# Performance work log

Hardware: AMD Instinct MI355X
Metric: run time of the kernel (lower is better)

## Reference

```python
import jax, jax.numpy as jnp
import numpy as np
import math

D = 128       # d_model (file-scope constant)
L_LEN = 128   # length; forced == d_model by the un-transposed attention call
NH = 4        # n_head
DK = D // NH
K = 7         # depthwise conv kernel size
LC = 4        # conv_num
EPS = 1e-5    # LayerNorm eps
NEG = -1e30


def _pos_encoding():
    i = np.arange(D).astype(np.float64)
    freqs = np.where(i % 2 == 0, 10000.0 ** (-i / D), -(10000.0 ** ((1 - i) / D)))
    phases = np.where(i % 2 == 0, 0.0, math.pi / 2)
    pos = np.arange(L_LEN).astype(np.float64)[None, :]          # (1, L)
    pe = np.sin(pos * freqs[:, None] + phases[:, None])          # (D, L)
    return jnp.asarray(pe, jnp.float32)

PE = _pos_encoding()


def layernorm2d(x, w, b):
    # LayerNorm over the trailing (D, L) dims jointly, elementwise affine (D, L)
    mu = x.mean(axis=(-2, -1), keepdims=True)
    var = x.var(axis=(-2, -1), keepdims=True)
    return (x - mu) * jax.lax.rsqrt(var + EPS) * w + b


def sep_conv(x, dw_w, dw_b, pw_w, pw_b):
    # depthwise conv1d (groups=C) then 1x1 pointwise conv. x: (B, C, L)
    h = jax.lax.conv_general_dilated(
        x, dw_w[:, None, :], window_strides=(1,), padding=[(K // 2, K // 2)],
        dimension_numbers=('NCH', 'OIH', 'NCH'), feature_group_count=D)
    h = h + dw_b[:, None]
    return jnp.einsum('bcl,oc->bol', h, pw_w) + pw_b[:, None]


def mha(x, mask_f, Wq, bq, Wk, bk, Wv, bv, Wo, bo):
    # x: (B, Lx, F) with Lx == F == D here (module feeds (B, d_model, length) untransposed)
    B, Lx, _ = x.shape
    q = (x @ Wq.T + bq).reshape(B, Lx, NH, DK)
    k = (x @ Wk.T + bk).reshape(B, Lx, NH, DK)
    v = (x @ Wv.T + bv).reshape(B, Lx, NH, DK)
    scores = jnp.einsum('bqhd,bkhd->bhqk', q, k) * (1.0 / math.sqrt(DK))
    m = mask_f[:, None, None, :]                         # (B,1,1,Lx)
    scores = scores * (1.0 - m) + m * NEG                # mask_logits
    attn = jax.nn.softmax(scores, axis=-1)
    out = jnp.einsum('bhqk,bkhd->bqhd', attn, v).reshape(B, Lx, D)
    return out @ Wo.T + bo


def setup_inputs() -> dict:
    key = jax.random.key(0)
    ks = jax.random.split(key, 16)
    B = 1024
    s = 0.02
    inp = {
        'x': jax.random.normal(ks[0], (B, D, L_LEN), jnp.float32),
        'mask': jax.random.randint(ks[1], (B, L_LEN), 0, 2, jnp.int32),
        'dw_w': jax.random.normal(ks[2], (LC, D, K), jnp.float32) * s,
        'dw_b': jnp.zeros((LC, D), jnp.float32),
        'pw_w': jax.random.normal(ks[3], (LC, D, D), jnp.float32) * s,
        'pw_b': jnp.zeros((LC, D), jnp.float32),
        'normb_w': jnp.ones((D, L_LEN), jnp.float32),
        'normb_b': jnp.zeros((D, L_LEN), jnp.float32),
        'norms_w': jnp.ones((LC, D, L_LEN), jnp.float32),
        'norms_b': jnp.zeros((LC, D, L_LEN), jnp.float32),
        'norme_w': jnp.ones((D, L_LEN), jnp.float32),
        'norme_b': jnp.zeros((D, L_LEN), jnp.float32),
        'Wq': jax.random.normal(ks[4], (D, D), jnp.float32) * s,
        'bq': jnp.zeros((D,), jnp.float32),
        'Wk': jax.random.normal(ks[5], (D, D), jnp.float32) * s,
        'bk': jnp.zeros((D,), jnp.float32),
        'Wv': jax.random.normal(ks[6], (D, D), jnp.float32) * s,
        'bv': jnp.zeros((D,), jnp.float32),
        'Wo': jax.random.normal(ks[7], (D, D), jnp.float32) * s,
        'bo': jnp.zeros((D,), jnp.float32),
        'fc_w': jax.random.normal(ks[8], (D, D), jnp.float32) * s,
        'fc_b': jnp.zeros((D,), jnp.float32),
    }
    return inp


def reference(x, mask, dw_w, dw_b, pw_w, pw_b, normb_w, normb_b, norms_w, norms_b,
              norme_w, norme_b, Wq, bq, Wk, bk, Wv, bv, Wo, bo, fc_w, fc_b):
    # Eval mode: all dropouts are identity.
    mask_f = mask.astype(x.dtype)
    out = x + PE                                  # PosEncoder
    res = out
    out = layernorm2d(out, normb_w, normb_b)      # normb
    for i in range(LC):                           # fixed small layer loop
        h = sep_conv(out, dw_w[i], dw_b[i], pw_w[i], pw_b[i])
        out = jax.nn.relu(h) + res
        res = out
        out = layernorm2d(out, norms_w[i], norms_b[i])
    att = mha(out, mask_f, Wq, bq, Wk, bk, Wv, bv, Wo, bo)
    out = att + res
    res = out
    out = layernorm2d(out, norme_w, norme_b)
    # fc applied over channel dim: (B,C,L)->(B,L,C) linear ->(B,C,L)
    h = jnp.einsum('bcl,oc->bol', out, fc_w) + fc_b[:, None]
    out = jax.nn.relu(h) + res
    return out
```

## Files before the change

kernel.cpp:

```cpp
#include <hip/hip_runtime.h>

#define NEGF -1e30f
#define EPSF 1e-5f

typedef __attribute__((ext_vector_type(8))) short bf16x8;
typedef __attribute__((ext_vector_type(4))) float f32x4;
typedef unsigned short u16;
typedef unsigned int u32;

#define WSU_PW 0
#define WSU_FC 65536
#define WSU_WO 81920
#define WSU_WQ 98304
#define WSU_WK 114688
#define WSU_WV 131072
#define WSU_END 147456

__device__ __forceinline__ u16 f2bf(float x) {
  u32 u = __float_as_uint(x);
  u += 0x7fffu + ((u >> 16) & 1u);
  return (u16)(u >> 16);
}
__device__ __forceinline__ float bf2f(u16 u) {
  return __uint_as_float(((u32)u) << 16);
}
__device__ __forceinline__ f32x4 mfma16(bf16x8 a, bf16x8 b, f32x4 c) {
  return __builtin_amdgcn_mfma_f32_16x16x32_bf16(a, b, c, 0, 0, 0);
}

__global__ __launch_bounds__(128) void prep_kernel(
    const float* __restrict__ pw_w, const float* __restrict__ fc_w,
    const float* __restrict__ Wo, const float* __restrict__ Wq,
    const float* __restrict__ Wk, const float* __restrict__ Wv,
    u16* __restrict__ wsu) {
  int job = blockIdx.x, r = blockIdx.y, c = threadIdx.x;
  int idx = r * 128 + c;
  if (job < 4)       wsu[WSU_PW + job * 16384 + idx] = f2bf(pw_w[job * 16384 + idx]);
  else if (job == 4) wsu[WSU_FC + idx] = f2bf(fc_w[idx]);
  else if (job == 5) wsu[WSU_WO + idx] = f2bf(Wo[idx]);
  else if (job == 6) wsu[WSU_WQ + idx] = f2bf(Wq[idx]);
  else if (job == 7) wsu[WSU_WK + idx] = f2bf(Wk[idx]);
  else if (job == 8) wsu[WSU_WV + idx] = f2bf(Wv[idx]);
  else {
    float* pe = (float*)(wsu + WSU_END);
    int d = r, pos = c;
    double freq, phase;
    if ((d & 1) == 0) { freq = pow(10000.0, -(double)d / 128.0); phase = 0.0; }
    else { freq = -pow(10000.0, (1.0 - (double)d) / 128.0); phase = 1.5707963267948966; }
    pe[d * 128 + pos] = (float)sin((double)pos * freq + phase);
  }
}

__device__ __forceinline__ void ln_stats(const float* resv, float* red, int t,
                                         float& mu, float& inv) {
  float s = 0.f, s2 = 0.f;
#pragma unroll
  for (int i = 0; i < 32; i++) { float v = resv[i]; s += v; s2 += v * v; }
#pragma unroll
  for (int off = 32; off > 0; off >>= 1) {
    s += __shfl_down(s, off, 64);
    s2 += __shfl_down(s2, off, 64);
  }
  if ((t & 63) == 0) { red[(t >> 6) * 2] = s; red[(t >> 6) * 2 + 1] = s2; }
  __syncthreads();
  float S = 0.f, S2 = 0.f;
#pragma unroll
  for (int i = 0; i < 8; i++) { S += red[2 * i]; S2 += red[2 * i + 1]; }
  mu = S * (1.0f / 16384.0f);
  float var = S2 * (1.0f / 16384.0f) - mu * mu;
  inv = rsqrtf(var + EPSF);
}

__global__ __launch_bounds__(512, 4) void enc_kernel(
    const float* __restrict__ x, const int* __restrict__ mask,
    const float* __restrict__ dw_w, const float* __restrict__ dw_b,
    const float* __restrict__ pw_b,
    const float* __restrict__ normb_w, const float* __restrict__ normb_b,
    const float* __restrict__ norms_w, const float* __restrict__ norms_b,
    const float* __restrict__ norme_w, const float* __restrict__ norme_b,
    const float* __restrict__ bq, const float* __restrict__ bk,
    const float* __restrict__ bv, const float* __restrict__ bo,
    const float* __restrict__ fc_b, const u16* __restrict__ wsu,
    const float* __restrict__ pe, float* __restrict__ out) {
  __shared__ __align__(16) u16 A_raw[128 * 136 + 16];
  __shared__ __align__(16) u16 B_[128 * 136];
  __shared__ float mask_s[128];
  __shared__ float red[16];
  u16* A = A_raw + 8;
  u16* QH = B_;
  u16* KH = B_ + 5120;
  u16* VT = B_ + 10240;
  u16* PN = B_;

  const int t = threadIdx.x;
  const int b = blockIdx.x;
  const int lane = t & 63;
  const int r16 = lane & 15;
  const int quad = lane >> 4;
  const int m0 = __builtin_amdgcn_readfirstlane((t >> 6) << 4);
  const int l = t & 127;
  const int obase = __builtin_amdgcn_readfirstlane((t >> 7) << 5);
  const int dw_o = t & 127;
  const int dw_seg = __builtin_amdgcn_readfirstlane(t >> 7);

  if (t < 128) mask_s[t] = (float)mask[b * 128 + t];

  float res[32];
  {
    const float* xb = x + (size_t)b * 16384;
#pragma unroll
    for (int i = 0; i < 32; i++) {
      int o = obase + i;
      res[i] = xb[o * 128 + l] + pe[o * 128 + l];
    }
  }
  {
    float mu, inv;
    ln_stats(res, red, t, mu, inv);
#pragma unroll
    for (int i = 0; i < 32; i++) {
      int o = obase + i;
      A[o * 136 + l] = f2bf((res[i] - mu) * inv * normb_w[o * 128 + l] + normb_b[o * 128 + l]);
    }
    __syncthreads();
  }

#pragma unroll 1
  for (int layer = 0; layer < 4; layer++) {
    {
      const float* dwp = dw_w + layer * 896 + dw_o * 7;
      float wreg[7];
#pragma unroll
      for (int j = 0; j < 7; j++) wreg[j] = dwp[j];
      float bias = dw_b[layer * 128 + dw_o];
      const u16* xrow = A + dw_o * 136;
#pragma unroll
      for (int k = 0; k < 4; k++) {
        const int lb = dw_seg * 32 + 8 * k;
        bf16x8 vz = {0, 0, 0, 0, 0, 0, 0, 0};
        bf16x8 vc = *(const bf16x8*)(xrow + lb);
        bf16x8 vp = (dw_seg == 0 && k == 0) ? vz : *(const bf16x8*)(xrow + lb - 8);
        bf16x8 vn = (dw_seg == 3 && k == 3) ? vz : *(const bf16x8*)(xrow + lb + 8);
        float w14[14];
        w14[0] = bf2f((u16)vp[5]); w14[1] = bf2f((u16)vp[6]); w14[2] = bf2f((u16)vp[7]);
#pragma unroll
        for (int j = 0; j < 8; j++) w14[3 + j] = bf2f((u16)vc[j]);
        w14[11] = bf2f((u16)vn[0]); w14[12] = bf2f((u16)vn[1]); w14[13] = bf2f((u16)vn[2]);
#pragma unroll
        for (int j = 0; j < 8; j++) {
          float a = bias;
#pragma unroll
          for (int tt = 0; tt < 7; tt++) a += w14[j + tt] * wreg[tt];
          B_[(lb + j) * 136 + dw_o] = f2bf(a);
        }
      }
    }
    __syncthreads();
    {
      const u16* pwp = wsu + WSU_PW + (layer << 14) + (m0 + r16) * 128 + quad * 8;
      bf16x8 a0 = *(const bf16x8*)(pwp);
      bf16x8 a1 = *(const bf16x8*)(pwp + 32);
      bf16x8 a2 = *(const bf16x8*)(pwp + 64);
      bf16x8 a3 = *(const bf16x8*)(pwp + 96);
#pragma unroll
      for (int n = 0; n < 8; n++) {
        const u16* hb = B_ + (16 * n + r16) * 136 + quad * 8;
        f32x4 c = {0.f, 0.f, 0.f, 0.f};
        c = mfma16(a0, *(const bf16x8*)(hb), c);
        c = mfma16(a1, *(const bf16x8*)(hb + 32), c);
        c = mfma16(a2, *(const bf16x8*)(hb + 64), c);
        c = mfma16(a3, *(const bf16x8*)(hb + 96), c);
        u16* sp = A + (m0 + quad * 4) * 136 + 16 * n + r16;
        sp[0] = f2bf(c[0]); sp[136] = f2bf(c[1]); sp[272] = f2bf(c[2]); sp[408] = f2bf(c[3]);
      }
    }
    __syncthreads();
    {
#pragma unroll
      for (int i = 0; i < 32; i++)
        res[i] += fmaxf(bf2f(A[(obase + i) * 136 + l]) + pw_b[layer * 128 + obase + i], 0.f);
      float mu, inv;
      ln_stats(res, red, t, mu, inv);
      const float* wg = norms_w + layer * 16384;
      const float* bg = norms_b + layer * 16384;
#pragma unroll
      for (int i = 0; i < 32; i++) {
        int o = obase + i;
        A[o * 136 + l] = f2bf((res[i] - mu) * inv * wg[o * 128 + l] + bg[o * 128 + l]);
      }
      __syncthreads();
    }
  }

  float att[32];
#pragma unroll
  for (int h = 0; h < 4; h++) {
    {
      const u16* xp = A + (m0 + r16) * 136 + quad * 8;
      bf16x8 x0 = *(const bf16x8*)(xp);
      bf16x8 x1 = *(const bf16x8*)(xp + 32);
      bf16x8 x2 = *(const bf16x8*)(xp + 64);
      bf16x8 x3 = *(const bf16x8*)(xp + 96);
#pragma unroll
      for (int n = 0; n < 2; n++) {
        const int jrow = 32 * h + 16 * n + r16;
        {
          const u16* wp = wsu + WSU_WQ + jrow * 128 + quad * 8;
          f32x4 c = {0.f, 0.f, 0.f, 0.f};
          c = mfma16(x0, *(const bf16x8*)(wp), c);
          c = mfma16(x1, *(const bf16x8*)(wp + 32), c);
          c = mfma16(x2, *(const bf16x8*)(wp + 64), c);
          c = mfma16(x3, *(const bf16x8*)(wp + 96), c);
          float bb = bq[jrow];
#pragma unroll
          for (int r = 0; r < 4; r++)
            QH[(m0 + quad * 4 + r) * 40 + 16 * n + r16] =
                f2bf((c[r] + bb) * 0.17677669529663687f);
        }
        {
          const u16* wp = wsu + WSU_WK + jrow * 128 + quad * 8;
          f32x4 c = {0.f, 0.f, 0.f, 0.f};
          c = mfma16(x0, *(const bf16x8*)(wp), c);
          c = mfma16(x1, *(const bf16x8*)(wp + 32), c);
          c = mfma16(x2, *(const bf16x8*)(wp + 64), c);
          c = mfma16(x3, *(const bf16x8*)(wp + 96), c);
          float bb = bk[jrow];
#pragma unroll
          for (int r = 0; r < 4; r++)
            KH[(m0 + quad * 4 + r) * 40 + 16 * n + r16] = f2bf(c[r] + bb);
        }
        {
          const u16* wp = wsu + WSU_WV + jrow * 128 + quad * 8;
          f32x4 c = {0.f, 0.f, 0.f, 0.f};
          c = mfma16(x0, *(const bf16x8*)(wp), c);
          c = mfma16(x1, *(const bf16x8*)(wp + 32), c);
          c = mfma16(x2, *(const bf16x8*)(wp + 64), c);
          c = mfma16(x3, *(const bf16x8*)(wp + 96), c);
          float bb = bv[jrow];
          u32 lo = (u32)f2bf(c[0] + bb) | ((u32)f2bf(c[1] + bb) << 16);
          u32 hi = (u32)f2bf(c[2] + bb) | ((u32)f2bf(c[3] + bb) << 16);
          u16* vp = VT + (16 * n + r16) * 136 + m0 + quad * 4;
          *(u32*)(vp) = lo;
          *(u32*)(vp + 2) = hi;
        }
      }
    }
    __syncthreads();
    f32x4 sc[8];
    {
      bf16x8 aq = *(const bf16x8*)(QH + (m0 + r16) * 40 + quad * 8);
#pragma unroll
      for (int n = 0; n < 8; n++) {
        f32x4 z = {0.f, 0.f, 0.f, 0.f};
        sc[n] = mfma16(aq, *(const bf16x8*)(KH + (16 * n + r16) * 40 + quad * 8), z);
      }
    }
    __syncthreads();
    float linv[4];
    u32 pk2[8];
    {
      float mv[8];
#pragma unroll
      for (int n = 0; n < 8; n++) mv[n] = mask_s[16 * n + r16];
#pragma unroll
      for (int r = 0; r < 4; r++) {
        float sv[8];
#pragma unroll
        for (int n = 0; n < 8; n++) sv[n] = (mv[n] > 0.5f) ? NEGF : sc[n][r];
        float mx = sv[0];
#pragma unroll
        for (int n = 1; n < 8; n++) mx = fmaxf(mx, sv[n]);
        mx = fmaxf(mx, __shfl_xor(mx, 1, 64));
        mx = fmaxf(mx, __shfl_xor(mx, 2, 64));
        mx = fmaxf(mx, __shfl_xor(mx, 4, 64));
        mx = fmaxf(mx, __shfl_xor(mx, 8, 64));
        float sum = 0.f;
#pragma unroll
        for (int n = 0; n < 8; n++) { float p = __expf(sv[n] - mx); sv[n] = p; sum += p; }
        sum += __shfl_xor(sum, 1, 64);
        sum += __shfl_xor(sum, 2, 64);
        sum += __shfl_xor(sum, 4, 64);
        sum += __shfl_xor(sum, 8, 64);
        linv[r] = 1.0f / sum;
        u16* pp = PN + (m0 + quad * 4 + r) * 72 + r16;
        pp[0] = f2bf(sv[0]); pp[16] = f2bf(sv[1]);
        pp[32] = f2bf(sv[2]); pp[48] = f2bf(sv[3]);
        pk2[r * 2 + 0] = (u32)f2bf(sv[4]) | ((u32)f2bf(sv[5]) << 16);
        pk2[r * 2 + 1] = (u32)f2bf(sv[6]) | ((u32)f2bf(sv[7]) << 16);
      }
    }
    f32x4 pv0 = {0.f, 0.f, 0.f, 0.f}, pv1 = {0.f, 0.f, 0.f, 0.f};
    {
      const u16* pq = PN + (m0 + r16) * 72 + quad * 8;
      bf16x8 p0 = *(const bf16x8*)(pq);
      bf16x8 p1 = *(const bf16x8*)(pq + 32);
      const u16* vb0 = VT + r16 * 136 + quad * 8;
      const u16* vb1 = VT + (16 + r16) * 136 + quad * 8;
      pv0 = mfma16(p0, *(const bf16x8*)(vb0), pv0);
      pv0 = mfma16(p1, *(const bf16x8*)(vb0 + 32), pv0);
      pv1 = mfma16(p0, *(const bf16x8*)(vb1), pv1);
      pv1 = mfma16(p1, *(const bf16x8*)(vb1 + 32), pv1);
#pragma unroll
      for (int r = 0; r < 4; r++) {
        u16* pp = PN + (m0 + quad * 4 + r) * 72 + r16;
        pp[0] = (u16)pk2[r * 2 + 0]; pp[16] = (u16)(pk2[r * 2 + 0] >> 16);
        pp[32] = (u16)pk2[r * 2 + 1]; pp[48] = (u16)(pk2[r * 2 + 1] >> 16);
      }
      bf16x8 p2 = *(const bf16x8*)(pq);
      bf16x8 p3 = *(const bf16x8*)(pq + 32);
      pv0 = mfma16(p2, *(const bf16x8*)(vb0 + 64), pv0);
      pv0 = mfma16(p3, *(const bf16x8*)(vb0 + 96), pv0);
      pv1 = mfma16(p2, *(const bf16x8*)(vb1 + 64), pv1);
      pv1 = mfma16(p3, *(const bf16x8*)(vb1 + 96), pv1);
    }
#pragma unroll
    for (int r = 0; r < 4; r++) {
      att[h * 8 + r] = pv0[r] * linv[r];
      att[h * 8 + 4 + r] = pv1[r] * linv[r];
    }
    __syncthreads();
  }

#pragma unroll
  for (int h = 0; h < 4; h++)
#pragma unroll
    for (int np = 0; np < 2; np++)
#pragma unroll
      for (int r = 0; r < 4; r++)
        A[(m0 + quad * 4 + r) * 136 + 32 * h + 16 * np + r16] =
            f2bf(att[h * 8 + np * 4 + r]);
  {
    const u16* ap = A + (m0 + r16) * 136 + quad * 8;
    bf16x8 a0 = *(const bf16x8*)(ap);
    bf16x8 a1 = *(const bf16x8*)(ap + 32);
    bf16x8 a2 = *(const bf16x8*)(ap + 64);
    bf16x8 a3 = *(const bf16x8*)(ap + 96);
#pragma unroll
    for (int n = 0; n < 8; n++) {
      const u16* wp = wsu + WSU_WO + (16 * n + r16) * 128 + quad * 8;
      f32x4 c = {0.f, 0.f, 0.f, 0.f};
      c = mfma16(a0, *(const bf16x8*)(wp), c);
      c = mfma16(a1, *(const bf16x8*)(wp + 32), c);
      c = mfma16(a2, *(const bf16x8*)(wp + 64), c);
      c = mfma16(a3, *(const bf16x8*)(wp + 96), c);
      u16* sp = B_ + (m0 + quad * 4) * 136 + 16 * n + r16;
      sp[0] = f2bf(c[0]); sp[136] = f2bf(c[1]); sp[272] = f2bf(c[2]); sp[408] = f2bf(c[3]);
    }
  }
  __syncthreads();
  {
    float bol = bo[l];
#pragma unroll
    for (int i = 0; i < 32; i++) res[i] += bf2f(B_[(obase + i) * 136 + l]) + bol;
    float mu, inv;
    ln_stats(res, red, t, mu, inv);
#pragma unroll
    for (int i = 0; i < 32; i += 2) {
      int o = obase + i;
      float v0 = (res[i] - mu) * inv * norme_w[o * 128 + l] + norme_b[o * 128 + l];
      float v1 = (res[i + 1] - mu) * inv * norme_w[(o + 1) * 128 + l] + norme_b[(o + 1) * 128 + l];
      *(u32*)(A + l * 136 + o) = (u32)f2bf(v0) | ((u32)f2bf(v1) << 16);
    }
    __syncthreads();
  }
  {
    const u16* fp = wsu + WSU_FC + (m0 + r16) * 128 + quad * 8;
    bf16x8 a0 = *(const bf16x8*)(fp);
    bf16x8 a1 = *(const bf16x8*)(fp + 32);
    bf16x8 a2 = *(const bf16x8*)(fp + 64);
    bf16x8 a3 = *(const bf16x8*)(fp + 96);
#pragma unroll
    for (int n = 0; n < 8; n++) {
      const u16* hb = A + (16 * n + r16) * 136 + quad * 8;
      f32x4 c = {0.f, 0.f, 0.f, 0.f};
      c = mfma16(a0, *(const bf16x8*)(hb), c);
      c = mfma16(a1, *(const bf16x8*)(hb + 32), c);
      c = mfma16(a2, *(const bf16x8*)(hb + 64), c);
      c = mfma16(a3, *(const bf16x8*)(hb + 96), c);
      u16* sp = B_ + (m0 + quad * 4) * 136 + 16 * n + r16;
      sp[0] = f2bf(c[0]); sp[136] = f2bf(c[1]); sp[272] = f2bf(c[2]); sp[408] = f2bf(c[3]);
    }
  }
  __syncthreads();
  {
    float* outb = out + (size_t)b * 16384;
#pragma unroll
    for (int i = 0; i < 32; i++) {
      float hv = bf2f(B_[(obase + i) * 136 + l]) + fc_b[obase + i];
      outb[(obase + i) * 128 + l] = fmaxf(hv, 0.f) + res[i];
    }
  }
}

extern "C" void kernel_launch(void* const* d_in, const int* in_sizes, int n_in,
                              void* d_out, int out_size, void* d_ws, size_t ws_size,
                              hipStream_t stream) {
  const float* x       = (const float*)d_in[0];
  const int*   mask    = (const int*)d_in[1];
  const float* dw_w    = (const float*)d_in[2];
  const float* dw_b    = (const float*)d_in[3];
  const float* pw_w    = (const float*)d_in[4];
  const float* pw_b    = (const float*)d_in[5];
  const float* normb_w = (const float*)d_in[6];
  const float* normb_b = (const float*)d_in[7];
  const float* norms_w = (const float*)d_in[8];
  const float* norms_b = (const float*)d_in[9];
  const float* norme_w = (const float*)d_in[10];
  const float* norme_b = (const float*)d_in[11];
  const float* Wq      = (const float*)d_in[12];
  const float* bq      = (const float*)d_in[13];
  const float* Wk      = (const float*)d_in[14];
  const float* bk      = (const float*)d_in[15];
  const float* Wv      = (const float*)d_in[16];
  const float* bv      = (const float*)d_in[17];
  const float* Wo      = (const float*)d_in[18];
  const float* bo      = (const float*)d_in[19];
  const float* fc_w    = (const float*)d_in[20];
  const float* fc_b    = (const float*)d_in[21];
  float* out = (float*)d_out;
  u16* wsu = (u16*)d_ws;
  const float* pe = (const float*)(wsu + WSU_END);
  int B = in_sizes[0] / 16384;

  prep_kernel<<<dim3(10, 128), dim3(128), 0, stream>>>(pw_w, fc_w, Wo, Wq, Wk, Wv, wsu);
  enc_kernel<<<dim3(B), dim3(512), 0, stream>>>(
      x, mask, dw_w, dw_b, pw_b, normb_w, normb_b, norms_w, norms_b,
      norme_w, norme_b, bq, bk, bv, bo, fc_b, wsu, pe, out);
}
```

Before: 678.2 us.

## Use 1024-thread blocks and process two attention heads per pass

Each batch element now gets 1024 threads instead of 512. Every wave handles half of the N tiles in the matmuls and half the rows in the elementwise and LayerNorm stages. Attention is restructured to compute Q/K/V for two heads at once (64 columns) and to run the full softmax row into PN before a single PV matmul, which removes the split P-store trick and halves the number of head passes. Shared memory for B_ grows to fit the wider Q/K/V buffers. The aim is more parallelism per block and fewer serialized head iterations, at the cost of fewer resident blocks per CU, larger LDS use and an extra barrier.

```diff
diff --git a/kernel.cpp b/kernel.cpp
--- a/kernel.cpp
+++ b/kernel.cpp
@@ -26,6 +26,12 @@
 }
 __device__ __forceinline__ f32x4 mfma16(bf16x8 a, bf16x8 b, f32x4 c) {
   return __builtin_amdgcn_mfma_f32_16x16x32_bf16(a, b, c, 0, 0, 0);
+}
+__device__ __forceinline__ void mm_frags(const u16* base, bf16x8* f) {
+  f[0] = *(const bf16x8*)(base);
+  f[1] = *(const bf16x8*)(base + 32);
+  f[2] = *(const bf16x8*)(base + 64);
+  f[3] = *(const bf16x8*)(base + 96);
 }
 
 __global__ __launch_bounds__(128) void prep_kernel(
@@ -55,7 +61,7 @@
                                          float& mu, float& inv) {
   float s = 0.f, s2 = 0.f;
 #pragma unroll
-  for (int i = 0; i < 32; i++) { float v = resv[i]; s += v; s2 += v * v; }
+  for (int i = 0; i < 16; i++) { float v = resv[i]; s += v; s2 += v * v; }
 #pragma unroll
   for (int off = 32; off > 0; off >>= 1) {
     s += __shfl_down(s, off, 64);
@@ -65,13 +71,13 @@
   __syncthreads();
   float S = 0.f, S2 = 0.f;
 #pragma unroll
-  for (int i = 0; i < 8; i++) { S += red[2 * i]; S2 += red[2 * i + 1]; }
+  for (int i = 0; i < 16; i++) { S += red[2 * i]; S2 += red[2 * i + 1]; }
   mu = S * (1.0f / 16384.0f);
   float var = S2 * (1.0f / 16384.0f) - mu * mu;
   inv = rsqrtf(var + EPSF);
 }
 
-__global__ __launch_bounds__(512, 4) void enc_kernel(
+__global__ __launch_bounds__(1024) void enc_kernel(
     const float* __restrict__ x, const int* __restrict__ mask,
     const float* __restrict__ dw_w, const float* __restrict__ dw_b,
     const float* __restrict__ pw_b,
@@ -83,13 +89,13 @@
     const float* __restrict__ fc_b, const u16* __restrict__ wsu,
     const float* __restrict__ pe, float* __restrict__ out) {
   __shared__ __align__(16) u16 A_raw[128 * 136 + 16];
-  __shared__ __align__(16) u16 B_[128 * 136];
+  __shared__ __align__(16) u16 B_[27136];
   __shared__ float mask_s[128];
-  __shared__ float red[16];
+  __shared__ float red[32];
   u16* A = A_raw + 8;
   u16* QH = B_;
-  u16* KH = B_ + 5120;
-  u16* VT = B_ + 10240;
+  u16* KH = B_ + 9216;
+  u16* VT = B_ + 18432;
   u16* PN = B_;
 
   const int t = threadIdx.x;
@@ -97,19 +103,22 @@
   const int lane = t & 63;
   const int r16 = lane & 15;
   const int quad = lane >> 4;
-  const int m0 = __builtin_amdgcn_readfirstlane((t >> 6) << 4);
+  const int wv = t >> 6;
+  const int m0 = __builtin_amdgcn_readfirstlane((wv >> 1) << 4);
+  const int nh = __builtin_amdgcn_readfirstlane(wv & 1);
   const int l = t & 127;
-  const int obase = __builtin_amdgcn_readfirstlane((t >> 7) << 5);
-  const int dw_o = t & 127;
-  const int dw_seg = __builtin_amdgcn_readfirstlane(t >> 7);
+  const int og = __builtin_amdgcn_readfirstlane(t >> 7);
+  const int obase = og << 4;
+  const int hh = __builtin_amdgcn_readfirstlane(wv >> 3);
+  const int mq0 = __builtin_amdgcn_readfirstlane((wv & 7) << 4);
 
   if (t < 128) mask_s[t] = (float)mask[b * 128 + t];
 
-  float res[32];
+  float res[16];
   {
     const float* xb = x + (size_t)b * 16384;
 #pragma unroll
-    for (int i = 0; i < 32; i++) {
+    for (int i = 0; i < 16; i++) {
       int o = obase + i;
       res[i] = xb[o * 128 + l] + pe[o * 128 + l];
     }
@@ -118,7 +127,7 @@
     float mu, inv;
     ln_stats(res, red, t, mu, inv);
 #pragma unroll
-    for (int i = 0; i < 32; i++) {
+    for (int i = 0; i < 16; i++) {
       int o = obase + i;
       A[o * 136 + l] = f2bf((res[i] - mu) * inv * normb_w[o * 128 + l] + normb_b[o * 128 + l]);
     }
@@ -128,19 +137,19 @@
 #pragma unroll 1
   for (int layer = 0; layer < 4; layer++) {
     {
-      const float* dwp = dw_w + layer * 896 + dw_o * 7;
+      const float* dwp = dw_w + layer * 896 + l * 7;
       float wreg[7];
 #pragma unroll
       for (int j = 0; j < 7; j++) wreg[j] = dwp[j];
-      float bias = dw_b[layer * 128 + dw_o];
-      const u16* xrow = A + dw_o * 136;
-#pragma unroll
-      for (int k = 0; k < 4; k++) {
-        const int lb = dw_seg * 32 + 8 * k;
+      float bias = dw_b[layer * 128 + l];
+      const u16* xrow = A + l * 136;
+#pragma unroll
+      for (int k = 0; k < 2; k++) {
+        const int lb = (og << 4) + 8 * k;
         bf16x8 vz = {0, 0, 0, 0, 0, 0, 0, 0};
         bf16x8 vc = *(const bf16x8*)(xrow + lb);
-        bf16x8 vp = (dw_seg == 0 && k == 0) ? vz : *(const bf16x8*)(xrow + lb - 8);
-        bf16x8 vn = (dw_seg == 3 && k == 3) ? vz : *(const bf16x8*)(xrow + lb + 8);
+        bf16x8 vp = (lb == 0) ? vz : *(const bf16x8*)(xrow + lb - 8);
+        bf16x8 vn = (lb == 120) ? vz : *(const bf16x8*)(xrow + lb + 8);
         float w14[14];
         w14[0] = bf2f((u16)vp[5]); w14[1] = bf2f((u16)vp[6]); w14[2] = bf2f((u16)vp[7]);
 #pragma unroll
@@ -151,25 +160,24 @@
           float a = bias;
 #pragma unroll
           for (int tt = 0; tt < 7; tt++) a += w14[j + tt] * wreg[tt];
-          B_[(lb + j) * 136 + dw_o] = f2bf(a);
+          B_[(lb + j) * 136 + l] = f2bf(a);
         }
       }
     }
     __syncthreads();
     {
       const u16* pwp = wsu + WSU_PW + (layer << 14) + (m0 + r16) * 128 + quad * 8;
-      bf16x8 a0 = *(const bf16x8*)(pwp);
-      bf16x8 a1 = *(const bf16x8*)(pwp + 32);
-      bf16x8 a2 = *(const bf16x8*)(pwp + 64);
-      bf16x8 a3 = *(const bf16x8*)(pwp + 96);
-#pragma unroll
-      for (int n = 0; n < 8; n++) {
+      bf16x8 a[4];
+      mm_frags(pwp, a);
+#pragma unroll
+      for (int ni = 0; ni < 4; ni++) {
+        int n = nh * 4 + ni;
         const u16* hb = B_ + (16 * n + r16) * 136 + quad * 8;
         f32x4 c = {0.f, 0.f, 0.f, 0.f};
-        c = mfma16(a0, *(const bf16x8*)(hb), c);
-        c = mfma16(a1, *(const bf16x8*)(hb + 32), c);
-        c = mfma16(a2, *(const bf16x8*)(hb + 64), c);
-        c = mfma16(a3, *(const bf16x8*)(hb + 96), c);
+        c = mfma16(a[0], *(const bf16x8*)(hb), c);
+        c = mfma16(a[1], *(const bf16x8*)(hb + 32), c);
+        c = mfma16(a[2], *(const bf16x8*)(hb + 64), c);
+        c = mfma16(a[3], *(const bf16x8*)(hb + 96), c);
         u16* sp = A + (m0 + quad * 4) * 136 + 16 * n + r16;
         sp[0] = f2bf(c[0]); sp[136] = f2bf(c[1]); sp[272] = f2bf(c[2]); sp[408] = f2bf(c[3]);
       }
@@ -177,14 +185,14 @@
     __syncthreads();
     {
 #pragma unroll
-      for (int i = 0; i < 32; i++)
+      for (int i = 0; i < 16; i++)
         res[i] += fmaxf(bf2f(A[(obase + i) * 136 + l]) + pw_b[layer * 128 + obase + i], 0.f);
       float mu, inv;
       ln_stats(res, red, t, mu, inv);
       const float* wg = norms_w + layer * 16384;
       const float* bg = norms_b + layer * 16384;
 #pragma unroll
-      for (int i = 0; i < 32; i++) {
+      for (int i = 0; i < 16; i++) {
         int o = obase + i;
         A[o * 136 + l] = f2bf((res[i] - mu) * inv * wg[o * 128 + l] + bg[o * 128 + l]);
       }
@@ -192,54 +200,50 @@
     }
   }
 
-  float att[32];
-#pragma unroll
-  for (int h = 0; h < 4; h++) {
+  float att[16];
+#pragma unroll
+  for (int p = 0; p < 2; p++) {
     {
       const u16* xp = A + (m0 + r16) * 136 + quad * 8;
-      bf16x8 x0 = *(const bf16x8*)(xp);
-      bf16x8 x1 = *(const bf16x8*)(xp + 32);
-      bf16x8 x2 = *(const bf16x8*)(xp + 64);
-      bf16x8 x3 = *(const bf16x8*)(xp + 96);
-#pragma unroll
-      for (int n = 0; n < 2; n++) {
-        const int jrow = 32 * h + 16 * n + r16;
+      bf16x8 xf[4];
+      mm_frags(xp, xf);
+#pragma unroll
+      for (int ni = 0; ni < 2; ni++) {
+        const int nt = nh * 2 + ni;
+        const int j2 = nt * 16 + r16;
+        const int jrow = p * 64 + j2;
         {
-          const u16* wp = wsu + WSU_WQ + jrow * 128 + quad * 8;
+          bf16x8 w[4];
+          mm_frags(wsu + WSU_WQ + jrow * 128 + quad * 8, w);
           f32x4 c = {0.f, 0.f, 0.f, 0.f};
-          c = mfma16(x0, *(const bf16x8*)(wp), c);
-          c = mfma16(x1, *(const bf16x8*)(wp + 32), c);
-          c = mfma16(x2, *(const bf16x8*)(wp + 64), c);
-          c = mfma16(x3, *(const bf16x8*)(wp + 96), c);
+          c = mfma16(xf[0], w[0], c); c = mfma16(xf[1], w[1], c);
+          c = mfma16(xf[2], w[2], c); c = mfma16(xf[3], w[3], c);
           float bb = bq[jrow];
 #pragma unroll
           for (int r = 0; r < 4; r++)
-            QH[(m0 + quad * 4 + r) * 40 + 16 * n + r16] =
-                f2bf((c[r] + bb) * 0.17677669529663687f);
+            QH[(m0 + quad * 4 + r) * 72 + j2] = f2bf((c[r] + bb) * 0.17677669529663687f);
         }
         {
-          const u16* wp = wsu + WSU_WK + jrow * 128 + quad * 8;
+          bf16x8 w[4];
+          mm_frags(wsu + WSU_WK + jrow * 128 + quad * 8, w);
           f32x4 c = {0.f, 0.f, 0.f, 0.f};
-          c = mfma16(x0, *(const bf16x8*)(wp), c);
-          c = mfma16(x1, *(const bf16x8*)(wp + 32), c);
-          c = mfma16(x2, *(const bf16x8*)(wp + 64), c);
-          c = mfma16(x3, *(const bf16x8*)(wp + 96), c);
+          c = mfma16(xf[0], w[0], c); c = mfma16(xf[1], w[1], c);
+          c = mfma16(xf[2], w[2], c); c = mfma16(xf[3], w[3], c);
           float bb = bk[jrow];
 #pragma unroll
           for (int r = 0; r < 4; r++)
-            KH[(m0 + quad * 4 + r) * 40 + 16 * n + r16] = f2bf(c[r] + bb);
+            KH[(m0 + quad * 4 + r) * 72 + j2] = f2bf(c[r] + bb);
         }
         {
-          const u16* wp = wsu + WSU_WV + jrow * 128 + quad * 8;
+          bf16x8 w[4];
+          mm_frags(wsu + WSU_WV + jrow * 128 + quad * 8, w);
           f32x4 c = {0.f, 0.f, 0.f, 0.f};
-          c = mfma16(x0, *(const bf16x8*)(wp), c);
-          c = mfma16(x1, *(const bf16x8*)(wp + 32), c);
-          c = mfma16(x2, *(const bf16x8*)(wp + 64), c);
-          c = mfma16(x3, *(const bf16x8*)(wp + 96), c);
+          c = mfma16(xf[0], w[0], c); c = mfma16(xf[1], w[1], c);
+          c = mfma16(xf[2], w[2], c); c = mfma16(xf[3], w[3], c);
           float bb = bv[jrow];
           u32 lo = (u32)f2bf(c[0] + bb) | ((u32)f2bf(c[1] + bb) << 16);
           u32 hi = (u32)f2bf(c[2] + bb) | ((u32)f2bf(c[3] + bb) << 16);
-          u16* vp = VT + (16 * n + r16) * 136 + m0 + quad * 4;
+          u16* vp = VT + j2 * 136 + m0 + quad * 4;
           *(u32*)(vp) = lo;
           *(u32*)(vp + 2) = hi;
         }
@@ -248,16 +252,15 @@
     __syncthreads();
     f32x4 sc[8];
     {
-      bf16x8 aq = *(const bf16x8*)(QH + (m0 + r16) * 40 + quad * 8);
+      bf16x8 aq = *(const bf16x8*)(QH + (mq0 + r16) * 72 + hh * 32 + quad * 8);
 #pragma unroll
       for (int n = 0; n < 8; n++) {
         f32x4 z = {0.f, 0.f, 0.f, 0.f};
-        sc[n] = mfma16(aq, *(const bf16x8*)(KH + (16 * n + r16) * 40 + quad * 8), z);
+        sc[n] = mfma16(aq, *(const bf16x8*)(KH + (16 * n + r16) * 72 + hh * 32 + quad * 8), z);
       }
     }
     __syncthreads();
     float linv[4];
-    u32 pk2[8];
     {
       float mv[8];
 #pragma unroll
@@ -276,73 +279,57 @@
         mx = fmaxf(mx, __shfl_xor(mx, 8, 64));
         float sum = 0.f;
 #pragma unroll
-        for (int n = 0; n < 8; n++) { float p = __expf(sv[n] - mx); sv[n] = p; sum += p; }
+        for (int n = 0; n < 8; n++) { float pp = __expf(sv[n] - mx); sv[n] = pp; sum += pp; }
         sum += __shfl_xor(sum, 1, 64);
         sum += __shfl_xor(sum, 2, 64);
         sum += __shfl_xor(sum, 4, 64);
         sum += __shfl_xor(sum, 8, 64);
         linv[r] = 1.0f / sum;
-        u16* pp = PN + (m0 + quad * 4 + r) * 72 + r16;
-        pp[0] = f2bf(sv[0]); pp[16] = f2bf(sv[1]);
-        pp[32] = f2bf(sv[2]); pp[48] = f2bf(sv[3]);
-        pk2[r * 2 + 0] = (u32)f2bf(sv[4]) | ((u32)f2bf(sv[5]) << 16);
-        pk2[r * 2 + 1] = (u32)f2bf(sv[6]) | ((u32)f2bf(sv[7]) << 16);
-      }
-    }
-    f32x4 pv0 = {0.f, 0.f, 0.f, 0.f}, pv1 = {0.f, 0.f, 0.f, 0.f};
-    {
-      const u16* pq = PN + (m0 + r16) * 72 + quad * 8;
-      bf16x8 p0 = *(const bf16x8*)(pq);
-      bf16x8 p1 = *(const bf16x8*)(pq + 32);
-      const u16* vb0 = VT + r16 * 136 + quad * 8;
-      const u16* vb1 = VT + (16 + r16) * 136 + quad * 8;
-      pv0 = mfma16(p0, *(const bf16x8*)(vb0), pv0);
-      pv0 = mfma16(p1, *(const bf16x8*)(vb0 + 32), pv0);
-      pv1 = mfma16(p0, *(const bf16x8*)(vb1), pv1);
-      pv1 = mfma16(p1, *(const bf16x8*)(vb1 + 32), pv1);
-#pragma unroll
-      for (int r = 0; r < 4; r++) {
-        u16* pp = PN + (m0 + quad * 4 + r) * 72 + r16;
-        pp[0] = (u16)pk2[r * 2 + 0]; pp[16] = (u16)(pk2[r * 2 + 0] >> 16);
-        pp[32] = (u16)pk2[r * 2 + 1]; pp[48] = (u16)(pk2[r * 2 + 1] >> 16);
-      }
-      bf16x8 p2 = *(const bf16x8*)(pq);
-      bf16x8 p3 = *(const bf16x8*)(pq + 32);
-      pv0 = mfma16(p2, *(const bf16x8*)(vb0 + 64), pv0);
-      pv0 = mfma16(p3, *(const bf16x8*)(vb0 + 96), pv0);
-      pv1 = mfma16(p2, *(const bf16x8*)(vb1 + 64), pv1);
-      pv1 = mfma16(p3, *(const bf16x8*)(vb1 + 96), pv1);
-    }
-#pragma unroll
-    for (int r = 0; r < 4; r++) {
-      att[h * 8 + r] = pv0[r] * linv[r];
-      att[h * 8 + 4 + r] = pv1[r] * linv[r];
-    }
-    __syncthreads();
-  }
-
-#pragma unroll
-  for (int h = 0; h < 4; h++)
-#pragma unroll
-    for (int np = 0; np < 2; np++)
+        u16* pp = PN + (mq0 + quad * 4 + r) * 136 + r16;
+#pragma unroll
+        for (int n = 0; n < 8; n++) pp[16 * n] = f2bf(sv[n]);
+      }
+    }
+    {
+      const u16* pq = PN + (mq0 + r16) * 136 + quad * 8;
+      bf16x8 pf[4];
+      mm_frags(pq, pf);
+#pragma unroll
+      for (int nv = 0; nv < 2; nv++) {
+        const u16* vb = VT + (hh * 32 + nv * 16 + r16) * 136 + quad * 8;
+        f32x4 c = {0.f, 0.f, 0.f, 0.f};
+        c = mfma16(pf[0], *(const bf16x8*)(vb), c);
+        c = mfma16(pf[1], *(const bf16x8*)(vb + 32), c);
+        c = mfma16(pf[2], *(const bf16x8*)(vb + 64), c);
+        c = mfma16(pf[3], *(const bf16x8*)(vb + 96), c);
+#pragma unroll
+        for (int r = 0; r < 4; r++) att[p * 8 + nv * 4 + r] = c[r] * linv[r];
+      }
+    }
+    __syncthreads();
+  }
+
+#pragma unroll
+  for (int p = 0; p < 2; p++)
+#pragma unroll
+    for (int nv = 0; nv < 2; nv++)
 #pragma unroll
       for (int r = 0; r < 4; r++)
-        A[(m0 + quad * 4 + r) * 136 + 32 * h + 16 * np + r16] =
-            f2bf(att[h * 8 + np * 4 + r]);
+        A[(mq0 + quad * 4 + r) * 136 + (2 * p + hh) * 32 + nv * 16 + r16] =
+            f2bf(att[p * 8 + nv * 4 + r]);
+  __syncthreads();
   {
     const u16* ap = A + (m0 + r16) * 136 + quad * 8;
-    bf16x8 a0 = *(const bf16x8*)(ap);
-    bf16x8 a1 = *(const bf16x8*)(ap + 32);
-    bf16x8 a2 = *(const bf16x8*)(ap + 64);
-    bf16x8 a3 = *(const bf16x8*)(ap + 96);
-#pragma unroll
-    for (int n = 0; n < 8; n++) {
-      const u16* wp = wsu + WSU_WO + (16 * n + r16) * 128 + quad * 8;
+    bf16x8 a[4];
+    mm_frags(ap, a);
+#pragma unroll
+    for (int ni = 0; ni < 4; ni++) {
+      int n = nh * 4 + ni;
+      bf16x8 w[4];
+      mm_frags(wsu + WSU_WO + (16 * n + r16) * 128 + quad * 8, w);
       f32x4 c = {0.f, 0.f, 0.f, 0.f};
-      c = mfma16(a0, *(const bf16x8*)(wp), c);
-      c = mfma16(a1, *(const bf16x8*)(wp + 32), c);
-      c = mfma16(a2, *(const bf16x8*)(wp + 64), c);
-      c = mfma16(a3, *(const bf16x8*)(wp + 96), c);
+      c = mfma16(a[0], w[0], c); c = mfma16(a[1], w[1], c);
+      c = mfma16(a[2], w[2], c); c = mfma16(a[3], w[3], c);
       u16* sp = B_ + (m0 + quad * 4) * 136 + 16 * n + r16;
       sp[0] = f2bf(c[0]); sp[136] = f2bf(c[1]); sp[272] = f2bf(c[2]); sp[408] = f2bf(c[3]);
     }
@@ -351,11 +338,11 @@
   {
     float bol = bo[l];
 #pragma unroll
-    for (int i = 0; i < 32; i++) res[i] += bf2f(B_[(obase + i) * 136 + l]) + bol;
+    for (int i = 0; i < 16; i++) res[i] += bf2f(B_[(obase + i) * 136 + l]) + bol;
     float mu, inv;
     ln_stats(res, red, t, mu, inv);
 #pragma unroll
-    for (int i = 0; i < 32; i += 2) {
+    for (int i = 0; i < 16; i += 2) {
       int o = obase + i;
       float v0 = (res[i] - mu) * inv * norme_w[o * 128 + l] + norme_b[o * 128 + l];
       float v1 = (res[i + 1] - mu) * inv * norme_w[(o + 1) * 128 + l] + norme_b[(o + 1) * 128 + l];
@@ -365,18 +352,17 @@
   }
   {
     const u16* fp = wsu + WSU_FC + (m0 + r16) * 128 + quad * 8;
-    bf16x8 a0 = *(const bf16x8*)(fp);
-    bf16x8 a1 = *(const bf16x8*)(fp + 32);
-    bf16x8 a2 = *(const bf16x8*)(fp + 64);
-    bf16x8 a3 = *(const bf16x8*)(fp + 96);
-#pragma unroll
-    for (int n = 0; n < 8; n++) {
+    bf16x8 a[4];
+    mm_frags(fp, a);
+#pragma unroll
+    for (int ni = 0; ni < 4; ni++) {
+      int n = nh * 4 + ni;
       const u16* hb = A + (16 * n + r16) * 136 + quad * 8;
       f32x4 c = {0.f, 0.f, 0.f, 0.f};
-      c = mfma16(a0, *(const bf16x8*)(hb), c);
-      c = mfma16(a1, *(const bf16x8*)(hb + 32), c);
-      c = mfma16(a2, *(const bf16x8*)(hb + 64), c);
-      c = mfma16(a3, *(const bf16x8*)(hb + 96), c);
+      c = mfma16(a[0], *(const bf16x8*)(hb), c);
+      c = mfma16(a[1], *(const bf16x8*)(hb + 32), c);
+      c = mfma16(a[2], *(const bf16x8*)(hb + 64), c);
+      c = mfma16(a[3], *(const bf16x8*)(hb + 96), c);
       u16* sp = B_ + (m0 + quad * 4) * 136 + 16 * n + r16;
       sp[0] = f2bf(c[0]); sp[136] = f2bf(c[1]); sp[272] = f2bf(c[2]); sp[408] = f2bf(c[3]);
     }
@@ -385,7 +371,7 @@
   {
     float* outb = out + (size_t)b * 16384;
 #pragma unroll
-    for (int i = 0; i < 32; i++) {
+    for (int i = 0; i < 16; i++) {
       float hv = bf2f(B_[(obase + i) * 136 + l]) + fc_b[obase + i];
       outb[(obase + i) * 128 + l] = fmaxf(hv, 0.f) + res[i];
     }
@@ -423,7 +409,7 @@
   int B = in_sizes[0] / 16384;
 
   prep_kernel<<<dim3(10, 128), dim3(128), 0, stream>>>(pw_w, fc_w, Wo, Wq, Wk, Wv, wsu);
-  enc_kernel<<<dim3(B), dim3(512), 0, stream>>>(
+  enc_kernel<<<dim3(B), dim3(1024), 0, stream>>>(
       x, mask, dw_w, dw_b, pw_b, normb_w, normb_b, norms_w, norms_b,
       norme_w, norme_b, bq, bk, bv, bo, fc_b, wsu, pe, out);
 }
```

After: 584.6 us. -13.8%, faster.
